# Kernel optimization log

Hardware: AMD Instinct MI355X
Metric: run time of the kernel (lower is better)

The kernel has to match this reference:

```python
import jax, jax.numpy as jnp
import numpy as np

HALF = 32          # (input_dim-1)//2
HIDDEN = 128
OUT_DIM = 10
B, T, C = 256, 512, 65


def setup_inputs() -> dict:
    key = jax.random.key(0)
    ks = jax.random.split(key, 20)
    s = 0.05
    gin = HALF + HIDDEN
    inp = {
        "times": jnp.arange(T, dtype=jnp.float32),
        "coeff_a": jax.random.normal(ks[0], (B, T - 1, C), jnp.float32),
        "coeff_b": jax.random.normal(ks[1], (B, T - 1, C), jnp.float32),
        "coeff_two_c": jax.random.normal(ks[2], (B, T - 1, C), jnp.float32),
        "coeff_three_d": jax.random.normal(ks[3], (B, T - 1, C), jnp.float32),
        "final_index": jax.random.randint(ks[4], (B,), 0, T),
        "Wr": jax.random.normal(ks[5], (gin, HIDDEN), jnp.float32) * s,
        "br": jnp.zeros((HIDDEN,), jnp.float32),
        "Wz": jax.random.normal(ks[6], (gin, HIDDEN), jnp.float32) * s,
        "bz": jnp.zeros((HIDDEN,), jnp.float32),
        "Wxn": jax.random.normal(ks[7], (HALF, HIDDEN), jnp.float32) * s,
        "bxn": jnp.zeros((HIDDEN,), jnp.float32),
        "Whn": jax.random.normal(ks[8], (HIDDEN, HIDDEN), jnp.float32) * s,
        "bhn": jnp.zeros((HIDDEN,), jnp.float32),
        "W_ode": jax.random.normal(ks[9], (HIDDEN, HIDDEN), jnp.float32) * s,
        "b_ode": jnp.zeros((HIDDEN,), jnp.float32),
        "W_lin": jax.random.normal(ks[10], (HIDDEN, OUT_DIM), jnp.float32) * s,
        "b_lin": jnp.zeros((OUT_DIM,), jnp.float32),
    }
    return inp


def _forward(times, coeff_a, coeff_b, coeff_two_c, coeff_three_d, final_index,
             Wr, br, Wz, bz, Wxn, bxn, Whn, bhn, W_ode, b_ode, W_lin, b_lin):
    maxlen = coeff_b.shape[-2] - 1

    def eval_spline(t):
        idx = jnp.clip(jnp.sum(t > times) - 1, 0, maxlen)
        fr = t - times[idx]
        inner = 0.5 * coeff_two_c[:, idx, :] + coeff_three_d[:, idx, :] * (fr / 3.0)
        inner = coeff_b[:, idx, :] + inner * fr
        return coeff_a[:, idx, :] + inner * fr  # [B, C]

    X = jax.vmap(eval_spline, out_axes=1)(times)  # [B, T, C]
    # difference the observation-indicator channels over time; make channel 0 a time delta
    X = X.at[:, 1:, 1:1 + HALF].add(-X[:, :-1, 1:1 + HALF])
    X = X.at[:, 0, 0].add(-times[0])
    X = X.at[:, 1:, 0].add(-times[:-1])

    nbatch = X.shape[0]

    def gru(x, h):
        comb = jnp.concatenate([x, h], axis=1)
        r = jax.nn.sigmoid(comb @ Wr + br)
        z = jax.nn.sigmoid(comb @ Wz + bz)
        n = jnp.tanh(x @ Wxn + bxn + (h @ Whn + bhn) * r)
        return (1.0 - z) * n + z * h

    def f_ode(h):
        return jnp.tanh(h @ W_ode + b_ode)

    def evolve(h, td):
        # single RK4 step from 0 to td
        k1 = f_ode(h)
        k2 = f_ode(h + 0.5 * td * k1)
        k3 = f_ode(h + 0.5 * td * k2)
        k4 = f_ode(h + td * k3)
        return h + (td / 6.0) * (k1 + 2.0 * k2 + 2.0 * k3 + k4)

    def step(h, dt, Xi):
        obs = jnp.max(Xi[:, 1:1 + HALF], axis=1) > 0.5
        Xp = Xi[:, 1 + HALF:].at[:, 0].add(dt)
        new_h = gru(Xp, h)

        def take(hd):
            h0, dt0 = hd
            return (jnp.where(obs[:, None], new_h, h0),
                    dt0 + jnp.where(obs, 0.0, Xi[:, 0]))

        return jax.lax.cond(jnp.any(obs), take, lambda hd: hd, (h, dt))

    z0 = jnp.zeros((nbatch, HIDDEN), X.dtype)
    dt0 = jnp.zeros((nbatch,), X.dtype)
    h0, dt0 = step(z0, dt0, X[:, 0])

    time_diffs = times[1:] - times[:-1]
    Xs = jnp.moveaxis(X[:, 1:], 1, 0)  # [T-1, B, C]

    def scan_body(carry, inp):
        h, dt = carry
        td, Xi = inp
        h = evolve(h, td)
        h, dt = step(h, dt, Xi)
        return (h, dt), h

    _, hs_rest = jax.lax.scan(scan_body, (h0, dt0), (time_diffs, Xs))
    out = jnp.concatenate([h0[:, None], jnp.moveaxis(hs_rest, 0, 1)], axis=1)  # [B, T, H]
    final = out[jnp.arange(nbatch), final_index]  # [B, H]
    return final @ W_lin + b_lin


def reference(times, coeff_a, coeff_b, coeff_two_c, coeff_three_d, final_index,
              Wr, br, Wz, bz, Wxn, bxn, Whn, bhn, W_ode, b_ode, W_lin, b_lin):
    return _forward(times, coeff_a, coeff_b, coeff_two_c, coeff_three_d, final_index,
                    Wr, br, Wz, bz, Wxn, bxn, Whn, bhn, W_ode, b_ode, W_lin, b_lin)
```

## Files before the change

### kernel.cpp

```cpp
#include <hip/hip_runtime.h>
#include <string.h>

#define TT 512
#define BB 256
#define CC 65
#define HALFC 32
#define HID 128
#define ODIM 10

typedef _Float16 half2_t __attribute__((ext_vector_type(2)));
typedef _Float16 half8_t __attribute__((ext_vector_type(8)));

__device__ __forceinline__ float ftanh(float x) {
  float u = __builtin_amdgcn_exp2f(x * -2.885390082f);
  return fmaf(2.f, __builtin_amdgcn_rcpf(1.f + u), -1.f);
}
__device__ __forceinline__ float fsig(float x) {
  float u = __builtin_amdgcn_exp2f(x * -1.442695041f);
  return __builtin_amdgcn_rcpf(1.f + u);
}

__device__ __forceinline__ half2_t h2cvt(float a, float b) {
  auto r = __builtin_amdgcn_cvt_pkrtz(a, b);
  half2_t o;
  memcpy(&o, &r, sizeof(o));
  return o;
}

__device__ __forceinline__ float fdot2h(half2_t a, half2_t b, float c) {
  return __builtin_amdgcn_fdot2(a, b, c, false);
}

template <int CTRL>
__device__ __forceinline__ float dpp_add(float x) {
  return x + __int_as_float(__builtin_amdgcn_update_dpp(
      0, __float_as_int(x), CTRL, 0xF, 0xF, true));
}
__device__ __forceinline__ float red4(float x) {
  x = dpp_add<0x101>(x);
  x = dpp_add<0x102>(x);
  return x;
}

__device__ __forceinline__ void block_sync_lds() {
  asm volatile("s_waitcnt lgkmcnt(0)" ::: "memory");
  __builtin_amdgcn_s_barrier();
  asm volatile("" ::: "memory");
}
__device__ __forceinline__ void vm_wait0() {
  asm volatile("s_waitcnt vmcnt(0)" ::: "memory");
}

__global__ void prep0(const float* __restrict__ times, float4* __restrict__ si,
                      int* __restrict__ anyobs) {
  __shared__ float ts[TT];
  int t = threadIdx.x;
  ts[t] = times[t];
  __syncthreads();
  float tv = ts[t];
  int cnt = 0;
  for (int jj = 0; jj < TT; ++jj) cnt += (tv > ts[jj]) ? 1 : 0;
  int idx = cnt - 1;
  idx = min(max(idx, 0), TT - 2);
  float4 o;
  o.x = __int_as_float(idx);
  o.y = tv - ts[idx];
  o.z = (t == 0) ? 0.f : (tv - ts[t - 1]);
  o.w = (t == 0) ? ts[0] : ts[t - 1];
  si[t] = o;
  anyobs[t] = 0;
}

__global__ void prep_obs(const float* __restrict__ ca, const float* __restrict__ cb,
                         const float* __restrict__ cc2, const float* __restrict__ cd,
                         const float4* __restrict__ si, int* __restrict__ anyobs,
                         unsigned char* __restrict__ obs) {
  int grp = blockIdx.x * (blockDim.x >> 5) + (threadIdx.x >> 5);
  int lane = threadIdx.x & 31;
  int t = grp & (TT - 1);
  int b = grp / TT;
  int ch = 1 + lane;
  float4 s = si[t];
  int idx = __float_as_int(s.x);
  float fr = s.y;
  size_t base = ((size_t)b * (TT - 1) + idx) * CC + ch;
  float f3 = fr / 3.f;
  float v = ca[base] + (cb[base] + (0.5f * cc2[base] + cd[base] * f3) * fr) * fr;
  float D = v;
  if (t >= 1) {
    float4 sp = si[t - 1];
    int idxp = __float_as_int(sp.x);
    float frp = sp.y;
    size_t basep = ((size_t)b * (TT - 1) + idxp) * CC + ch;
    float f3p = frp / 3.f;
    float vp = ca[basep] + (cb[basep] + (0.5f * cc2[basep] + cd[basep] * f3p) * frp) * frp;
    D = v - vp;
  }
  float m = D;
  #pragma unroll
  for (int off = 16; off >= 1; off >>= 1) m = fmaxf(m, __shfl_xor(m, off));
  if (lane == 0) {
    unsigned char o = (m > 0.5f) ? (unsigned char)1 : (unsigned char)0;
    obs[(size_t)b * TT + t] = o;
    if (o) atomicOr(&anyobs[t], 1);
  }
}

__launch_bounds__(256, 1)
__global__ void ode_main(
    const float* __restrict__ ca, const float* __restrict__ cb,
    const float* __restrict__ cc2, const float* __restrict__ cd,
    const int* __restrict__ final_index,
    const float* __restrict__ Wr, const float* __restrict__ br,
    const float* __restrict__ Wz, const float* __restrict__ bz,
    const float* __restrict__ Wxn, const float* __restrict__ bxn,
    const float* __restrict__ Whn, const float* __restrict__ bhn,
    const float* __restrict__ Wode, const float* __restrict__ bode,
    const float* __restrict__ Wlin, const float* __restrict__ blin,
    const float4* __restrict__ si, const int* __restrict__ anyobs,
    const unsigned char* __restrict__ obsArr,
    float* __restrict__ out)
{
  __shared__ alignas(16) half2_t hS2[HID / 2];
  __shared__ alignas(16) half2_t vA2[HID / 2];
  __shared__ alignas(16) half2_t vB2[HID / 2];
  __shared__ alignas(16) _Float16 xh[HALFC];
  __shared__ float xs0f;
  __shared__ alignas(16) float4 siL[TT];
  __shared__ unsigned char flagL[TT];

  const int tid = threadIdx.x;
  const int b = blockIdx.x;
  const int lane = tid & 63;
  const int wv = tid >> 6;
  const int p = lane >> 2;
  const int kk = lane & 3;
  const int s = wv * 16 + p;
  const int j0 = 2 * s;
  const int wbyte = 4 * s;

  half2_t wodeH[32], whnH[32], wrhH[32], wzhH[32];
  #pragma unroll
  for (int i = 0; i < 16; ++i) {
    const int r0 = 32 * kk + 2 * i, r1 = r0 + 1;
    float2 q0, q1;
    q0 = *(const float2*)&Wode[r0 * HID + j0];
    q1 = *(const float2*)&Wode[r1 * HID + j0];
    wodeH[2*i] = h2cvt(q0.x, q1.x); wodeH[2*i+1] = h2cvt(q0.y, q1.y);
    q0 = *(const float2*)&Whn[r0 * HID + j0];
    q1 = *(const float2*)&Whn[r1 * HID + j0];
    whnH[2*i] = h2cvt(q0.x, q1.x); whnH[2*i+1] = h2cvt(q0.y, q1.y);
    q0 = *(const float2*)&Wr[(HALFC + r0) * HID + j0];
    q1 = *(const float2*)&Wr[(HALFC + r1) * HID + j0];
    wrhH[2*i] = h2cvt(q0.x, q1.x); wrhH[2*i+1] = h2cvt(q0.y, q1.y);
    q0 = *(const float2*)&Wz[(HALFC + r0) * HID + j0];
    q1 = *(const float2*)&Wz[(HALFC + r1) * HID + j0];
    wzhH[2*i] = h2cvt(q0.x, q1.x); wzhH[2*i+1] = h2cvt(q0.y, q1.y);
  }
  half2_t wrxH[8], wzxH[8], wxnH[8];
  #pragma unroll
  for (int i = 0; i < 4; ++i) {
    const int c0 = 8 * kk + 2 * i, c1 = c0 + 1;
    float2 q0, q1;
    q0 = *(const float2*)&Wr[c0 * HID + j0];
    q1 = *(const float2*)&Wr[c1 * HID + j0];
    wrxH[i] = h2cvt(q0.x, q1.x); wrxH[4+i] = h2cvt(q0.y, q1.y);
    q0 = *(const float2*)&Wz[c0 * HID + j0];
    q1 = *(const float2*)&Wz[c1 * HID + j0];
    wzxH[i] = h2cvt(q0.x, q1.x); wzxH[4+i] = h2cvt(q0.y, q1.y);
    q0 = *(const float2*)&Wxn[c0 * HID + j0];
    q1 = *(const float2*)&Wxn[c1 * HID + j0];
    wxnH[i] = h2cvt(q0.x, q1.x); wxnH[4+i] = h2cvt(q0.y, q1.y);
  }
  float wr0a = 0.f, wr0b = 0.f, wz0a = 0.f, wz0b = 0.f, wx0a = 0.f, wx0b = 0.f;
  if (kk == 0) {
    wrxH[0][0] = (_Float16)0.f; wrxH[4][0] = (_Float16)0.f;
    wzxH[0][0] = (_Float16)0.f; wzxH[4][0] = (_Float16)0.f;
    wxnH[0][0] = (_Float16)0.f; wxnH[4][0] = (_Float16)0.f;
    wr0a = Wr[j0];  wr0b = Wr[j0 + 1];
    wz0a = Wz[j0];  wz0b = Wz[j0 + 1];
    wx0a = Wxn[j0]; wx0b = Wxn[j0 + 1];
  }
  float bo0, bo1, bh0, bh1, br0, br1, bz0, bz1, bx0, bx1;
  { float2 q;
    q = *(const float2*)&bode[j0]; bo0 = q.x; bo1 = q.y;
    q = *(const float2*)&bhn [j0]; bh0 = q.x; bh1 = q.y;
    q = *(const float2*)&br  [j0]; br0 = q.x; br1 = q.y;
    q = *(const float2*)&bz  [j0]; bz0 = q.x; bz1 = q.y;
    q = *(const float2*)&bxn [j0]; bx0 = q.x; bx1 = q.y;
  }
  const int fidx = final_index[b];

  #pragma unroll
  for (int it = 0; it < 2; ++it) {
    const int tt = tid + it * 256;
    siL[tt] = si[tt];
    const int ao = anyobs[tt];
    const unsigned char o = obsArr[(size_t)b * TT + tt];
    flagL[tt] = (unsigned char)((ao ? 1 : 0) | (o ? 2 : 0));
  }
  if (tid < HID / 2) {
    const half2_t z2 = {(_Float16)0.f, (_Float16)0.f};
    hS2[tid] = z2; vA2[tid] = z2; vB2[tid] = z2;
  }
  if (tid < HALFC) xh[tid] = (_Float16)0.f;
  if (tid == 0) xs0f = 0.f;
  float hj0 = 0.f, hj1 = 0.f;
  float dtv = 0.f;
  block_sync_lds();

  auto mv = [&](const half2_t* __restrict__ buf, const half2_t (&w)[32],
                float& o0, float& o1) {
    half2_t v2[16];
    #pragma unroll
    for (int q = 0; q < 4; ++q) {
      const half8_t x8 = *(const half8_t*)((const char*)buf + 64 * kk + 16 * q);
      v2[4*q+0] = __builtin_shufflevector(x8, x8, 0, 1);
      v2[4*q+1] = __builtin_shufflevector(x8, x8, 2, 3);
      v2[4*q+2] = __builtin_shufflevector(x8, x8, 4, 5);
      v2[4*q+3] = __builtin_shufflevector(x8, x8, 6, 7);
    }
    float a0 = 0.f, a1 = 0.f, b0 = 0.f, b1 = 0.f;
    #pragma unroll
    for (int i = 0; i < 8; ++i) {
      a0 = fdot2h(v2[i],     w[2*i],       a0);
      a1 = fdot2h(v2[i],     w[2*i+1],     a1);
      b0 = fdot2h(v2[8 + i], w[2*(8+i)],   b0);
      b1 = fdot2h(v2[8 + i], w[2*(8+i)+1], b1);
    }
    o0 = red4(a0 + b0);
    o1 = red4(a1 + b1);
  };

  const int xch = wv * 8 + lane;
  const bool xlane = (lane < 8);

  float4 sv4 = siL[0];
  int flg = flagL[0];

  float xa = 0.f, xb = 0.f, xc = 0.f, xd = 0.f;
  float ya = 0.f, yb = 0.f, yc = 0.f, yd = 0.f;
  if (xlane) {
    const size_t base = ((size_t)b * (TT - 1) + __float_as_int(sv4.x)) * CC;
    const int ch = 33 + xch;
    xa = ca[base + ch]; xb = cb[base + ch]; xc = cc2[base + ch]; xd = cd[base + ch];
    if (tid == 0) { ya = ca[base]; yb = cb[base]; yc = cc2[base]; yd = cd[base]; }
  }

  for (int t = 0; ; ++t) {
    const float fr = sv4.y, td = sv4.z, tsub = sv4.w;
    const bool doGru = (flg & 2) != 0;

    float xdelta = 0.f;
    vm_wait0();
    if (xlane) {
      const float f3 = fr * (1.f / 3.f);
      float sv = xa + (xb + (0.5f * xc + xd * f3) * fr) * fr;
      if (tid == 0) {
        const float s0 = ya + (yb + (0.5f * yc + yd * f3) * fr) * fr;
        xdelta = s0 - tsub;
        sv += dtv;
        xs0f = sv;
      }
      xh[xch] = (_Float16)sv;
    }

    const int tn = (t < TT - 1) ? t + 1 : t;
    const float4 sv4N = siL[tn];
    const int flgN = flagL[tn];
    if (xlane) {
      const size_t base = ((size_t)b * (TT - 1) + __float_as_int(sv4N.x)) * CC;
      const int ch = 33 + xch;
      xa = ca[base + ch]; xb = cb[base + ch]; xc = cc2[base + ch]; xd = cd[base + ch];
      if (tid == 0) { ya = ca[base]; yb = cb[base]; yc = cc2[base]; yd = cd[base]; }
    }

    float rxp0 = 0.f, rxp1 = 0.f, zxp0 = 0.f, zxp1 = 0.f, xxp0 = 0.f, xxp1 = 0.f;

    if (t > 0) {
      const float htd = 0.5f * td;
      float p0, p1, k0, k1, ks0, ks1;
      mv(hS2, wodeH, p0, p1);
      k0 = ftanh(p0 + bo0); k1 = ftanh(p1 + bo1);
      ks0 = k0; ks1 = k1;
      if (kk == 0)
        *(half2_t*)((char*)vA2 + wbyte) =
            h2cvt(fmaf(htd, k0, hj0), fmaf(htd, k1, hj1));
      block_sync_lds();
      if (doGru) {
        const half8_t x8 = *(const half8_t*)((const char*)xh + 16 * kk);
        half2_t xv2[4];
        xv2[0] = __builtin_shufflevector(x8, x8, 0, 1);
        xv2[1] = __builtin_shufflevector(x8, x8, 2, 3);
        xv2[2] = __builtin_shufflevector(x8, x8, 4, 5);
        xv2[3] = __builtin_shufflevector(x8, x8, 6, 7);
        #pragma unroll
        for (int i = 0; i < 4; ++i) {
          rxp0 = fdot2h(xv2[i], wrxH[i],   rxp0);
          rxp1 = fdot2h(xv2[i], wrxH[4+i], rxp1);
          zxp0 = fdot2h(xv2[i], wzxH[i],   zxp0);
          zxp1 = fdot2h(xv2[i], wzxH[4+i], zxp1);
          xxp0 = fdot2h(xv2[i], wxnH[i],   xxp0);
          xxp1 = fdot2h(xv2[i], wxnH[4+i], xxp1);
        }
        if (kk == 0) {
          const float x0 = xs0f;
          rxp0 = fmaf(x0, wr0a, rxp0); rxp1 = fmaf(x0, wr0b, rxp1);
          zxp0 = fmaf(x0, wz0a, zxp0); zxp1 = fmaf(x0, wz0b, zxp1);
          xxp0 = fmaf(x0, wx0a, xxp0); xxp1 = fmaf(x0, wx0b, xxp1);
        }
      }
      mv(vA2, wodeH, p0, p1);
      k0 = ftanh(p0 + bo0); k1 = ftanh(p1 + bo1);
      ks0 = fmaf(2.f, k0, ks0); ks1 = fmaf(2.f, k1, ks1);
      if (kk == 0)
        *(half2_t*)((char*)vB2 + wbyte) =
            h2cvt(fmaf(htd, k0, hj0), fmaf(htd, k1, hj1));
      block_sync_lds();
      mv(vB2, wodeH, p0, p1);
      k0 = ftanh(p0 + bo0); k1 = ftanh(p1 + bo1);
      ks0 = fmaf(2.f, k0, ks0); ks1 = fmaf(2.f, k1, ks1);
      if (kk == 0)
        *(half2_t*)((char*)vA2 + wbyte) =
            h2cvt(fmaf(td, k0, hj0), fmaf(td, k1, hj1));
      block_sync_lds();
      mv(vA2, wodeH, p0, p1);
      k0 = ftanh(p0 + bo0); k1 = ftanh(p1 + bo1);
      ks0 += k0; ks1 += k1;
      hj0 = fmaf(td * (1.f / 6.f), ks0, hj0);
      hj1 = fmaf(td * (1.f / 6.f), ks1, hj1);
      if (kk == 0)
        *(half2_t*)((char*)vB2 + wbyte) = h2cvt(hj0, hj1);
      block_sync_lds();
    } else {
      block_sync_lds();
      if (doGru) {
        const half8_t x8 = *(const half8_t*)((const char*)xh + 16 * kk);
        half2_t xv2[4];
        xv2[0] = __builtin_shufflevector(x8, x8, 0, 1);
        xv2[1] = __builtin_shufflevector(x8, x8, 2, 3);
        xv2[2] = __builtin_shufflevector(x8, x8, 4, 5);
        xv2[3] = __builtin_shufflevector(x8, x8, 6, 7);
        #pragma unroll
        for (int i = 0; i < 4; ++i) {
          rxp0 = fdot2h(xv2[i], wrxH[i],   rxp0);
          rxp1 = fdot2h(xv2[i], wrxH[4+i], rxp1);
          zxp0 = fdot2h(xv2[i], wzxH[i],   zxp0);
          zxp1 = fdot2h(xv2[i], wzxH[4+i], zxp1);
          xxp0 = fdot2h(xv2[i], wxnH[i],   xxp0);
          xxp1 = fdot2h(xv2[i], wxnH[4+i], xxp1);
        }
        if (kk == 0) {
          const float x0 = xs0f;
          rxp0 = fmaf(x0, wr0a, rxp0); rxp1 = fmaf(x0, wr0b, rxp1);
          zxp0 = fmaf(x0, wz0a, zxp0); zxp1 = fmaf(x0, wz0b, zxp1);
          xxp0 = fmaf(x0, wx0a, xxp0); xxp1 = fmaf(x0, wx0b, xxp1);
        }
      }
    }

    if (doGru) {
      half2_t v2[16];
      #pragma unroll
      for (int q = 0; q < 4; ++q) {
        const half8_t x8 = *(const half8_t*)((const char*)vB2 + 64 * kk + 16 * q);
        v2[4*q+0] = __builtin_shufflevector(x8, x8, 0, 1);
        v2[4*q+1] = __builtin_shufflevector(x8, x8, 2, 3);
        v2[4*q+2] = __builtin_shufflevector(x8, x8, 4, 5);
        v2[4*q+3] = __builtin_shufflevector(x8, x8, 6, 7);
      }
      float rp0 = rxp0, rp1 = rxp1, zp0 = zxp0, zp1 = zxp1;
      float gp0 = 0.f, gp1 = 0.f, xp0 = xxp0, xp1 = xxp1;
      #pragma unroll
      for (int i = 0; i < 16; ++i) {
        rp0 = fdot2h(v2[i], wrhH[2*i],   rp0);
        rp1 = fdot2h(v2[i], wrhH[2*i+1], rp1);
        zp0 = fdot2h(v2[i], wzhH[2*i],   zp0);
        zp1 = fdot2h(v2[i], wzhH[2*i+1], zp1);
        gp0 = fdot2h(v2[i], whnH[2*i],   gp0);
        gp1 = fdot2h(v2[i], whnH[2*i+1], gp1);
      }
      rp0 = red4(rp0); rp1 = red4(rp1);
      zp0 = red4(zp0); zp1 = red4(zp1);
      gp0 = red4(gp0); gp1 = red4(gp1);
      xp0 = red4(xp0); xp1 = red4(xp1);
      const float r0 = fsig(rp0 + br0), r1 = fsig(rp1 + br1);
      const float z0 = fsig(zp0 + bz0), z1 = fsig(zp1 + bz1);
      const float n0 = ftanh(xp0 + bx0 + (gp0 + bh0) * r0);
      const float n1 = ftanh(xp1 + bx1 + (gp1 + bh1) * r1);
      hj0 = fmaf(z0, hj0 - n0, n0);
      hj1 = fmaf(z1, hj1 - n1, n1);
      if (kk == 0)
        *(half2_t*)((char*)hS2 + wbyte) = h2cvt(hj0, hj1);
    } else {
      if (tid == 0 && (flg & 1)) dtv += xdelta;
    }

    if (t == fidx) break;
    sv4 = sv4N;
    flg = flgN;
    if (doGru) block_sync_lds();
  }

  block_sync_lds();
  if (tid < ODIM) {
    float acc = blin[tid];
    const _Float16* hf = (const _Float16*)hS2;
    #pragma unroll 8
    for (int q = 0; q < HID; ++q) {
      const float hv = (float)hf[q];
      acc = fmaf(hv, Wlin[q * ODIM + tid], acc);
    }
    out[b * ODIM + tid] = acc;
  }
}

extern "C" void kernel_launch(void* const* d_in, const int* in_sizes, int n_in,
                              void* d_out, int out_size, void* d_ws, size_t ws_size,
                              hipStream_t stream) {
  const float* times = (const float*)d_in[0];
  const float* ca   = (const float*)d_in[1];
  const float* cb   = (const float*)d_in[2];
  const float* cc2  = (const float*)d_in[3];
  const float* cd   = (const float*)d_in[4];
  const int*   fidx = (const int*)d_in[5];
  const float* Wr   = (const float*)d_in[6];
  const float* br   = (const float*)d_in[7];
  const float* Wz   = (const float*)d_in[8];
  const float* bz   = (const float*)d_in[9];
  const float* Wxn  = (const float*)d_in[10];
  const float* bxn  = (const float*)d_in[11];
  const float* Whn  = (const float*)d_in[12];
  const float* bhn  = (const float*)d_in[13];
  const float* Wode = (const float*)d_in[14];
  const float* bode = (const float*)d_in[15];
  const float* Wlin = (const float*)d_in[16];
  const float* blin = (const float*)d_in[17];
  float* out = (float*)d_out;

  char* ws = (char*)d_ws;
  float4* si = (float4*)ws;
  int* anyobs = (int*)(ws + TT * 16);
  unsigned char* obs = (unsigned char*)(ws + TT * 16 + TT * 4);

  prep0<<<1, TT, 0, stream>>>(times, si, anyobs);
  prep_obs<<<(BB * TT) / 8, 256, 0, stream>>>(ca, cb, cc2, cd, si, anyobs, obs);
  ode_main<<<BB, 256, 0, stream>>>(ca, cb, cc2, cd, fidx, Wr, br, Wz, bz,
                                   Wxn, bxn, Whn, bhn, Wode, bode, Wlin, blin,
                                   si, anyobs, obs, out);
}
```

Measured before the change: 904.9 us.

## Halve ode_main block to 128 threads with 2-lane dot-product splits

Remaps the recurrent kernel so each pair of hidden outputs is computed by 2 lanes instead of 4. The block shrinks from 4 waves to 2, and each lane holds twice as many fp16 weight registers. The aim is cheaper barriers and a shorter DPP reduction on the latency-bound per-timestep path. In exchange, each lane runs twice as many serial fdot2 operations. Register pressure roughly doubles, which risks spilling.

```diff
diff --git a/kernel.cpp b/kernel.cpp
--- a/kernel.cpp
+++ b/kernel.cpp
@@ -36,10 +36,8 @@
   return x + __int_as_float(__builtin_amdgcn_update_dpp(
       0, __float_as_int(x), CTRL, 0xF, 0xF, true));
 }
-__device__ __forceinline__ float red4(float x) {
-  x = dpp_add<0x101>(x);
-  x = dpp_add<0x102>(x);
-  return x;
+__device__ __forceinline__ float red2(float x) {
+  return dpp_add<0x101>(x);
 }
 
 __device__ __forceinline__ void block_sync_lds() {
@@ -106,7 +104,7 @@
   }
 }
 
-__launch_bounds__(256, 1)
+__launch_bounds__(128, 1)
 __global__ void ode_main(
     const float* __restrict__ ca, const float* __restrict__ cb,
     const float* __restrict__ cc2, const float* __restrict__ cd,
@@ -133,16 +131,16 @@
   const int b = blockIdx.x;
   const int lane = tid & 63;
   const int wv = tid >> 6;
-  const int p = lane >> 2;
-  const int kk = lane & 3;
-  const int s = wv * 16 + p;
+  const int p = lane >> 1;
+  const int kk = lane & 1;
+  const int s = wv * 32 + p;
   const int j0 = 2 * s;
   const int wbyte = 4 * s;
 
-  half2_t wodeH[32], whnH[32], wrhH[32], wzhH[32];
+  half2_t wodeH[64], whnH[64], wrhH[64], wzhH[64];
   #pragma unroll
-  for (int i = 0; i < 16; ++i) {
-    const int r0 = 32 * kk + 2 * i, r1 = r0 + 1;
+  for (int i = 0; i < 32; ++i) {
+    const int r0 = 64 * kk + 2 * i, r1 = r0 + 1;
     float2 q0, q1;
     q0 = *(const float2*)&Wode[r0 * HID + j0];
     q1 = *(const float2*)&Wode[r1 * HID + j0];
@@ -157,26 +155,26 @@
     q1 = *(const float2*)&Wz[(HALFC + r1) * HID + j0];
     wzhH[2*i] = h2cvt(q0.x, q1.x); wzhH[2*i+1] = h2cvt(q0.y, q1.y);
   }
-  half2_t wrxH[8], wzxH[8], wxnH[8];
+  half2_t wrxH[16], wzxH[16], wxnH[16];
   #pragma unroll
-  for (int i = 0; i < 4; ++i) {
-    const int c0 = 8 * kk + 2 * i, c1 = c0 + 1;
+  for (int i = 0; i < 8; ++i) {
+    const int c0 = 16 * kk + 2 * i, c1 = c0 + 1;
     float2 q0, q1;
     q0 = *(const float2*)&Wr[c0 * HID + j0];
     q1 = *(const float2*)&Wr[c1 * HID + j0];
-    wrxH[i] = h2cvt(q0.x, q1.x); wrxH[4+i] = h2cvt(q0.y, q1.y);
+    wrxH[i] = h2cvt(q0.x, q1.x); wrxH[8+i] = h2cvt(q0.y, q1.y);
     q0 = *(const float2*)&Wz[c0 * HID + j0];
     q1 = *(const float2*)&Wz[c1 * HID + j0];
-    wzxH[i] = h2cvt(q0.x, q1.x); wzxH[4+i] = h2cvt(q0.y, q1.y);
+    wzxH[i] = h2cvt(q0.x, q1.x); wzxH[8+i] = h2cvt(q0.y, q1.y);
     q0 = *(const float2*)&Wxn[c0 * HID + j0];
     q1 = *(const float2*)&Wxn[c1 * HID + j0];
-    wxnH[i] = h2cvt(q0.x, q1.x); wxnH[4+i] = h2cvt(q0.y, q1.y);
+    wxnH[i] = h2cvt(q0.x, q1.x); wxnH[8+i] = h2cvt(q0.y, q1.y);
   }
   float wr0a = 0.f, wr0b = 0.f, wz0a = 0.f, wz0b = 0.f, wx0a = 0.f, wx0b = 0.f;
   if (kk == 0) {
-    wrxH[0][0] = (_Float16)0.f; wrxH[4][0] = (_Float16)0.f;
-    wzxH[0][0] = (_Float16)0.f; wzxH[4][0] = (_Float16)0.f;
-    wxnH[0][0] = (_Float16)0.f; wxnH[4][0] = (_Float16)0.f;
+    wrxH[0][0] = (_Float16)0.f; wrxH[8][0] = (_Float16)0.f;
+    wzxH[0][0] = (_Float16)0.f; wzxH[8][0] = (_Float16)0.f;
+    wxnH[0][0] = (_Float16)0.f; wxnH[8][0] = (_Float16)0.f;
     wr0a = Wr[j0];  wr0b = Wr[j0 + 1];
     wz0a = Wz[j0];  wz0b = Wz[j0 + 1];
     wx0a = Wxn[j0]; wx0b = Wxn[j0 + 1];
@@ -192,8 +190,8 @@
   const int fidx = final_index[b];
 
   #pragma unroll
-  for (int it = 0; it < 2; ++it) {
-    const int tt = tid + it * 256;
+  for (int it = 0; it < 4; ++it) {
+    const int tt = tid + it * 128;
     siL[tt] = si[tt];
     const int ao = anyobs[tt];
     const unsigned char o = obsArr[(size_t)b * TT + tt];
@@ -209,12 +207,12 @@
   float dtv = 0.f;
   block_sync_lds();
 
-  auto mv = [&](const half2_t* __restrict__ buf, const half2_t (&w)[32],
+  auto mv = [&](const half2_t* __restrict__ buf, const half2_t (&w)[64],
                 float& o0, float& o1) {
-    half2_t v2[16];
+    half2_t v2[32];
     #pragma unroll
-    for (int q = 0; q < 4; ++q) {
-      const half8_t x8 = *(const half8_t*)((const char*)buf + 64 * kk + 16 * q);
+    for (int q = 0; q < 8; ++q) {
+      const half8_t x8 = *(const half8_t*)((const char*)buf + 128 * kk + 16 * q);
       v2[4*q+0] = __builtin_shufflevector(x8, x8, 0, 1);
       v2[4*q+1] = __builtin_shufflevector(x8, x8, 2, 3);
       v2[4*q+2] = __builtin_shufflevector(x8, x8, 4, 5);
@@ -222,18 +220,18 @@
     }
     float a0 = 0.f, a1 = 0.f, b0 = 0.f, b1 = 0.f;
     #pragma unroll
-    for (int i = 0; i < 8; ++i) {
-      a0 = fdot2h(v2[i],     w[2*i],       a0);
-      a1 = fdot2h(v2[i],     w[2*i+1],     a1);
-      b0 = fdot2h(v2[8 + i], w[2*(8+i)],   b0);
-      b1 = fdot2h(v2[8 + i], w[2*(8+i)+1], b1);
-    }
-    o0 = red4(a0 + b0);
-    o1 = red4(a1 + b1);
+    for (int i = 0; i < 16; ++i) {
+      a0 = fdot2h(v2[i],      w[2*i],        a0);
+      a1 = fdot2h(v2[i],      w[2*i+1],      a1);
+      b0 = fdot2h(v2[16 + i], w[2*(16+i)],   b0);
+      b1 = fdot2h(v2[16 + i], w[2*(16+i)+1], b1);
+    }
+    o0 = red2(a0 + b0);
+    o1 = red2(a1 + b1);
   };
 
-  const int xch = wv * 8 + lane;
-  const bool xlane = (lane < 8);
+  const int xch = wv * 16 + lane;
+  const bool xlane = (lane < 16);
 
   float4 sv4 = siL[0];
   int flg = flagL[0];
@@ -277,6 +275,33 @@
 
     float rxp0 = 0.f, rxp1 = 0.f, zxp0 = 0.f, zxp1 = 0.f, xxp0 = 0.f, xxp1 = 0.f;
 
+    auto xpartials = [&]() {
+      half2_t xv2[8];
+      #pragma unroll
+      for (int q = 0; q < 2; ++q) {
+        const half8_t x8 = *(const half8_t*)((const char*)xh + 32 * kk + 16 * q);
+        xv2[4*q+0] = __builtin_shufflevector(x8, x8, 0, 1);
+        xv2[4*q+1] = __builtin_shufflevector(x8, x8, 2, 3);
+        xv2[4*q+2] = __builtin_shufflevector(x8, x8, 4, 5);
+        xv2[4*q+3] = __builtin_shufflevector(x8, x8, 6, 7);
+      }
+      #pragma unroll
+      for (int i = 0; i < 8; ++i) {
+        rxp0 = fdot2h(xv2[i], wrxH[i],   rxp0);
+        rxp1 = fdot2h(xv2[i], wrxH[8+i], rxp1);
+        zxp0 = fdot2h(xv2[i], wzxH[i],   zxp0);
+        zxp1 = fdot2h(xv2[i], wzxH[8+i], zxp1);
+        xxp0 = fdot2h(xv2[i], wxnH[i],   xxp0);
+        xxp1 = fdot2h(xv2[i], wxnH[8+i], xxp1);
+      }
+      if (kk == 0) {
+        const float x0 = xs0f;
+        rxp0 = fmaf(x0, wr0a, rxp0); rxp1 = fmaf(x0, wr0b, rxp1);
+        zxp0 = fmaf(x0, wz0a, zxp0); zxp1 = fmaf(x0, wz0b, zxp1);
+        xxp0 = fmaf(x0, wx0a, xxp0); xxp1 = fmaf(x0, wx0b, xxp1);
+      }
+    };
+
     if (t > 0) {
       const float htd = 0.5f * td;
       float p0, p1, k0, k1, ks0, ks1;
@@ -287,29 +312,7 @@
         *(half2_t*)((char*)vA2 + wbyte) =
             h2cvt(fmaf(htd, k0, hj0), fmaf(htd, k1, hj1));
       block_sync_lds();
-      if (doGru) {
-        const half8_t x8 = *(const half8_t*)((const char*)xh + 16 * kk);
-        half2_t xv2[4];
-        xv2[0] = __builtin_shufflevector(x8, x8, 0, 1);
-        xv2[1] = __builtin_shufflevector(x8, x8, 2, 3);
-        xv2[2] = __builtin_shufflevector(x8, x8, 4, 5);
-        xv2[3] = __builtin_shufflevector(x8, x8, 6, 7);
-        #pragma unroll
-        for (int i = 0; i < 4; ++i) {
-          rxp0 = fdot2h(xv2[i], wrxH[i],   rxp0);
-          rxp1 = fdot2h(xv2[i], wrxH[4+i], rxp1);
-          zxp0 = fdot2h(xv2[i], wzxH[i],   zxp0);
-          zxp1 = fdot2h(xv2[i], wzxH[4+i], zxp1);
-          xxp0 = fdot2h(xv2[i], wxnH[i],   xxp0);
-          xxp1 = fdot2h(xv2[i], wxnH[4+i], xxp1);
-        }
-        if (kk == 0) {
-          const float x0 = xs0f;
-          rxp0 = fmaf(x0, wr0a, rxp0); rxp1 = fmaf(x0, wr0b, rxp1);
-          zxp0 = fmaf(x0, wz0a, zxp0); zxp1 = fmaf(x0, wz0b, zxp1);
-          xxp0 = fmaf(x0, wx0a, xxp0); xxp1 = fmaf(x0, wx0b, xxp1);
-        }
-      }
+      if (doGru) xpartials();
       mv(vA2, wodeH, p0, p1);
       k0 = ftanh(p0 + bo0); k1 = ftanh(p1 + bo1);
       ks0 = fmaf(2.f, k0, ks0); ks1 = fmaf(2.f, k1, ks1);
@@ -334,36 +337,14 @@
       block_sync_lds();
     } else {
       block_sync_lds();
-      if (doGru) {
-        const half8_t x8 = *(const half8_t*)((const char*)xh + 16 * kk);
-        half2_t xv2[4];
-        xv2[0] = __builtin_shufflevector(x8, x8, 0, 1);
-        xv2[1] = __builtin_shufflevector(x8, x8, 2, 3);
-        xv2[2] = __builtin_shufflevector(x8, x8, 4, 5);
-        xv2[3] = __builtin_shufflevector(x8, x8, 6, 7);
-        #pragma unroll
-        for (int i = 0; i < 4; ++i) {
-          rxp0 = fdot2h(xv2[i], wrxH[i],   rxp0);
-          rxp1 = fdot2h(xv2[i], wrxH[4+i], rxp1);
-          zxp0 = fdot2h(xv2[i], wzxH[i],   zxp0);
-          zxp1 = fdot2h(xv2[i], wzxH[4+i], zxp1);
-          xxp0 = fdot2h(xv2[i], wxnH[i],   xxp0);
-          xxp1 = fdot2h(xv2[i], wxnH[4+i], xxp1);
-        }
-        if (kk == 0) {
-          const float x0 = xs0f;
-          rxp0 = fmaf(x0, wr0a, rxp0); rxp1 = fmaf(x0, wr0b, rxp1);
-          zxp0 = fmaf(x0, wz0a, zxp0); zxp1 = fmaf(x0, wz0b, zxp1);
-          xxp0 = fmaf(x0, wx0a, xxp0); xxp1 = fmaf(x0, wx0b, xxp1);
-        }
-      }
+      if (doGru) xpartials();
     }
 
     if (doGru) {
-      half2_t v2[16];
+      half2_t v2[32];
       #pragma unroll
-      for (int q = 0; q < 4; ++q) {
-        const half8_t x8 = *(const half8_t*)((const char*)vB2 + 64 * kk + 16 * q);
+      for (int q = 0; q < 8; ++q) {
+        const half8_t x8 = *(const half8_t*)((const char*)vB2 + 128 * kk + 16 * q);
         v2[4*q+0] = __builtin_shufflevector(x8, x8, 0, 1);
         v2[4*q+1] = __builtin_shufflevector(x8, x8, 2, 3);
         v2[4*q+2] = __builtin_shufflevector(x8, x8, 4, 5);
@@ -372,7 +353,7 @@
       float rp0 = rxp0, rp1 = rxp1, zp0 = zxp0, zp1 = zxp1;
       float gp0 = 0.f, gp1 = 0.f, xp0 = xxp0, xp1 = xxp1;
       #pragma unroll
-      for (int i = 0; i < 16; ++i) {
+      for (int i = 0; i < 32; ++i) {
         rp0 = fdot2h(v2[i], wrhH[2*i],   rp0);
         rp1 = fdot2h(v2[i], wrhH[2*i+1], rp1);
         zp0 = fdot2h(v2[i], wzhH[2*i],   zp0);
@@ -380,10 +361,10 @@
         gp0 = fdot2h(v2[i], whnH[2*i],   gp0);
         gp1 = fdot2h(v2[i], whnH[2*i+1], gp1);
       }
-      rp0 = red4(rp0); rp1 = red4(rp1);
-      zp0 = red4(zp0); zp1 = red4(zp1);
-      gp0 = red4(gp0); gp1 = red4(gp1);
-      xp0 = red4(xp0); xp1 = red4(xp1);
+      rp0 = red2(rp0); rp1 = red2(rp1);
+      zp0 = red2(zp0); zp1 = red2(zp1);
+      gp0 = red2(gp0); gp1 = red2(gp1);
+      xp0 = red2(xp0); xp1 = red2(xp1);
       const float r0 = fsig(rp0 + br0), r1 = fsig(rp1 + br1);
       const float z0 = fsig(zp0 + bz0), z1 = fsig(zp1 + bz1);
       const float n0 = ftanh(xp0 + bx0 + (gp0 + bh0) * r0);
@@ -445,7 +426,7 @@
 
   prep0<<<1, TT, 0, stream>>>(times, si, anyobs);
   prep_obs<<<(BB * TT) / 8, 256, 0, stream>>>(ca, cb, cc2, cd, si, anyobs, obs);
-  ode_main<<<BB, 256, 0, stream>>>(ca, cb, cc2, cd, fidx, Wr, br, Wz, bz,
+  ode_main<<<BB, 128, 0, stream>>>(ca, cb, cc2, cd, fidx, Wr, br, Wz, bz,
                                    Wxn, bxn, Whn, bhn, Wode, bode, Wlin, blin,
                                    si, anyobs, obs, out);
 }
```

After: 1.236 ms. 36.5% more time.
